# Performance work log

Measured on AMD Instinct MI355X. Metric: run time of the kernel, lower is better.

The kernel has to match this reference:

```python
import jax, jax.numpy as jnp
import numpy as np
from functools import partial

N_SEEDS = 1000       # n
BG_LOW, BG_UP = 0.3, 0.7
ERODE_K, ERODE_ITER = 11, 1
KSZ = 3
IGNORE = -255
INT_MAX = np.iinfo(np.int32).max


def _min_pool2d(x, k):
    # binary erosion with a kxk all-ones structuring element, SAME padding
    return jax.lax.reduce_window(x, INT_MAX, jax.lax.min, (k, k), (1, 1), 'SAME')


def _max_pool3d(x, k):
    # binary dilation over (B,H,W) with kxk window on spatial dims
    return jax.lax.reduce_window(x, -INT_MAX, jax.lax.max, (1, k, k), (1, 1, 1), 'SAME')


def _otsu_threshold(flat255):
    # flat255: int32 pixel values in [0,255]
    hist = jnp.zeros(256, jnp.float32).at[flat255].add(1.0)
    total = jnp.asarray(flat255.shape[0], jnp.float32)
    bins = jnp.arange(256, dtype=jnp.float32)
    w = jnp.cumsum(hist)                 # class-0 pixel count up to bin t
    m = jnp.cumsum(hist * bins)          # class-0 intensity mass up to t
    mT = m[-1]
    denom = w * (total - w)
    sigma_b = jnp.where(denom > 0, (mT * w - total * m) ** 2 / (denom * total * total), 0.0)
    th = jnp.argmax(sigma_b).astype(jnp.float32)
    bad = jnp.sum(hist > 0) <= 1         # degenerate histogram -> bad_egg
    return th, bad


def _sample_mask(eligible, key, hw):
    # uniform sampling without replacement of min(N_SEEDS, #eligible)
    # via random-score top-k restricted to eligible positions
    scores = jnp.where(eligible, jax.random.uniform(key, (hw,)), -jnp.inf)
    vals, idx = jax.lax.top_k(scores, N_SEEDS)
    sel = (vals > -jnp.inf).astype(jnp.int32)
    return jnp.zeros(hw, jnp.int32).at[idx].max(sel)


def _one_sample(cam, key):
    h, w = cam.shape
    hw = h * w
    cam255 = jnp.floor(cam * 255.0)
    flat255 = jnp.clip(cam255.astype(jnp.int32).ravel(), 0, 255)

    th, bad = _otsu_threshold(flat255)
    th = jnp.where(bad, jnp.median(cam * 255.0), th)
    th = jnp.where(th == 0, 1.0, jnp.where(th == 255, 254.0, th))

    roi = (cam255 > th).astype(jnp.int32)
    for _ in range(ERODE_ITER):
        roi = _min_pool2d(roi, ERODE_K)

    kf, kb, kz = jax.random.split(key, 3)
    # foreground: sample uniformly from eroded ROI pixels
    fg = _sample_mask(roi.ravel() == 1, kf, hw)
    # background: sample uniformly from the nbr_bg lowest-activation pixels
    z = jax.random.uniform(kz, (), minval=BG_LOW, maxval=BG_UP)
    nbr_bg = jnp.ceil(z * hw)
    order = jnp.argsort(cam.ravel())
    rank = jnp.zeros(hw, jnp.int32).at[order].set(jnp.arange(hw, dtype=jnp.int32))
    bg = _sample_mask(rank.astype(jnp.float32) < nbr_bg, kb, hw)
    return fg.reshape(h, w), bg.reshape(h, w)


def setup_inputs() -> dict:
    key = jax.random.key(0)
    x = jax.random.uniform(key, (128, 1, 512, 512), dtype=jnp.float32)
    return {"x": x}


def reference(x):
    b, d, h, w = x.shape
    keys = jax.random.split(jax.random.key(42), b)
    all_fg, all_bg = jax.vmap(_one_sample)(x[:, 0], keys)   # (B,H,W) int32
    # dilation with ksz x ksz ones kernel
    all_fg = _max_pool3d(all_fg, KSZ)
    all_bg = _max_pool3d(all_bg, KSZ)
    outer = all_fg + all_bg
    all_fg = jnp.where(outer == 2, 0, all_fg)
    all_bg = jnp.where(outer == 2, 0, all_bg)
    out = jnp.full((b, h, w), IGNORE, dtype=jnp.int32)
    out = jnp.where(all_fg == 1, 1, out)
    out = jnp.where(all_bg == 1, 0, out)
    return out
```

## Files before the change

kernel.cpp:

```cpp
#include <hip/hip_runtime.h>
#include <cstdint>

typedef unsigned short u16;

constexpr int BATCH = 128;
constexpr int H = 512, W = 512;
constexpr int HW = H * W;
constexpr int WPR = W / 64;
constexpr int WPI = HW / 64;
constexpr int NSEED = 1000;
constexpr int MARGIN = 3000;
constexpr int CAP2 = 4096;
constexpr int CAPS = 1024;
constexpr int LBUF = 2048;
constexpr int NBIN = 4096;
constexpr int QSEG = 128;

__device__ __forceinline__ uint32_t rotl32(uint32_t v, int d) {
  return (v << d) | (v >> (32 - d));
}

__device__ __forceinline__ void tf2x32(uint32_t k0, uint32_t k1,
                                       uint32_t x0, uint32_t x1,
                                       uint32_t &o0, uint32_t &o1) {
  uint32_t ks2 = k0 ^ k1 ^ 0x1BD11BDAu;
  x0 += k0; x1 += k1;
  x0 += x1; x1 = rotl32(x1, 13); x1 ^= x0;
  x0 += x1; x1 = rotl32(x1, 15); x1 ^= x0;
  x0 += x1; x1 = rotl32(x1, 26); x1 ^= x0;
  x0 += x1; x1 = rotl32(x1, 6);  x1 ^= x0;
  x0 += k1; x1 += ks2 + 1u;
  x0 += x1; x1 = rotl32(x1, 17); x1 ^= x0;
  x0 += x1; x1 = rotl32(x1, 29); x1 ^= x0;
  x0 += x1; x1 = rotl32(x1, 16); x1 ^= x0;
  x0 += x1; x1 = rotl32(x1, 24); x1 ^= x0;
  x0 += ks2; x1 += k0 + 2u;
  x0 += x1; x1 = rotl32(x1, 13); x1 ^= x0;
  x0 += x1; x1 = rotl32(x1, 15); x1 ^= x0;
  x0 += x1; x1 = rotl32(x1, 26); x1 ^= x0;
  x0 += x1; x1 = rotl32(x1, 6);  x1 ^= x0;
  x0 += k0; x1 += k1 + 3u;
  x0 += x1; x1 = rotl32(x1, 17); x1 ^= x0;
  x0 += x1; x1 = rotl32(x1, 29); x1 ^= x0;
  x0 += x1; x1 = rotl32(x1, 16); x1 ^= x0;
  x0 += x1; x1 = rotl32(x1, 24); x1 ^= x0;
  x0 += k1; x1 += ks2 + 4u;
  x0 += x1; x1 = rotl32(x1, 13); x1 ^= x0;
  x0 += x1; x1 = rotl32(x1, 15); x1 ^= x0;
  x0 += x1; x1 = rotl32(x1, 26); x1 ^= x0;
  x0 += x1; x1 = rotl32(x1, 6);  x1 ^= x0;
  x0 += ks2; x1 += k0 + 5u;
  o0 = x0; o1 = x1;
}

__device__ __forceinline__ uint32_t score_bits(uint32_t k0, uint32_t k1, uint32_t i) {
  uint32_t a, c; tf2x32(k0, k1, 0u, i, a, c);
  return a ^ c;
}

__device__ __forceinline__ void keygen(int b, uint32_t* keys, uint32_t* kbg,
                                       uint32_t* Tbg) {
  uint32_t kb0, kb1; tf2x32(0u, 42u, 0u, (uint32_t)b, kb0, kb1);
  uint32_t kf0, kf1; tf2x32(kb0, kb1, 0u, 0u, kf0, kf1);
  uint32_t kB0, kB1; tf2x32(kb0, kb1, 0u, 1u, kB0, kB1);
  uint32_t kz0, kz1; tf2x32(kb0, kb1, 0u, 2u, kz0, kz1);
  uint32_t za, zc; tf2x32(kz0, kz1, 0u, 0u, za, zc);
  uint32_t zb = za ^ zc;
  keys[b * 4 + 0] = kf0; keys[b * 4 + 1] = kf1;
  keys[b * 4 + 2] = kB0; keys[b * 4 + 3] = kB1;
  float uu = __uint_as_float((zb >> 9) | 0x3f800000u) - 1.0f;
  float span = __fsub_rn(0.7f, 0.3f);
  float z = __fadd_rn(__fmul_rn(uu, span), 0.3f);
  z = fmaxf(0.3f, z);
  float nb = ceilf(__fmul_rn(z, (float)HW));
  uint32_t K = (uint32_t)nb;
  kbg[b] = K;
  float tv = floorf((1.0f - (float)MARGIN / (float)K) * 8388608.0f);
  Tbg[b] = (uint32_t)fmaxf(tv, 0.0f);
}

__global__ __launch_bounds__(1024) void k_binify(const float4* __restrict__ x4,
                                                 u16* __restrict__ g,
                                                 uint32_t* __restrict__ gh,
                                                 uint32_t* __restrict__ keys,
                                                 uint32_t* __restrict__ kbg,
                                                 uint32_t* __restrict__ Tbg,
                                                 uint32_t* __restrict__ Efg,
                                                 uint32_t* __restrict__ cnt_fg,
                                                 uint32_t* __restrict__ cnt_be,
                                                 uint32_t* __restrict__ cnt_bg) {
  __shared__ uint32_t h[NBIN];
  int b = blockIdx.x >> 2, sub = blockIdx.x & 3, t = threadIdx.x;
  if (blockIdx.x == 0 && t < BATCH) {
    keygen(t, keys, kbg, Tbg);
    Efg[t] = 0; cnt_fg[t] = 0; cnt_be[t] = 0; cnt_bg[t] = 0;
  }
  for (int i = t; i < NBIN; i += 1024) h[i] = 0;
  __syncthreads();
  const float4* xb = x4 + ((size_t)b * HW + (size_t)sub * (HW / 4)) / 4;
  ushort4* gb4 = (ushort4*)g + ((size_t)b * HW + (size_t)sub * (HW / 4)) / 4;
  for (int i = t; i < HW / 16; i += 1024) {
    float4 v4 = xb[i];
    int g0 = (int)floorf(__fmul_rn(v4.x, 4080.0f)); g0 = min(max(g0, 0), 4079);
    int g1 = (int)floorf(__fmul_rn(v4.y, 4080.0f)); g1 = min(max(g1, 0), 4079);
    int g2 = (int)floorf(__fmul_rn(v4.z, 4080.0f)); g2 = min(max(g2, 0), 4079);
    int g3 = (int)floorf(__fmul_rn(v4.w, 4080.0f)); g3 = min(max(g3, 0), 4079);
    atomicAdd(&h[g0], 1u);
    atomicAdd(&h[g1], 1u);
    atomicAdd(&h[g2], 1u);
    atomicAdd(&h[g3], 1u);
    ushort4 o;
    o.x = (u16)g0; o.y = (u16)g1; o.z = (u16)g2; o.w = (u16)g3;
    gb4[i] = o;
  }
  __syncthreads();
  uint32_t* dst = gh + ((size_t)blockIdx.x << 12);
  for (int i = t; i < NBIN; i += 1024) dst[i] = h[i];
}

__device__ __forceinline__ void lds_tree_cumsum256x2(float* Lc, float* Sc,
                                                     float* Lm, float* Sm, int tid) {
  const int off[9] = {0, 256, 384, 448, 480, 496, 504, 508, 510};
  const int sz[9]  = {256, 128, 64, 32, 16, 8, 4, 2, 1};
  for (int l = 0; l < 8; ++l) {
    int o = off[l], on = off[l + 1], n = sz[l + 1];
    if (tid < n) {
      Lc[on + tid] = __fadd_rn(Lc[o + 2 * tid], Lc[o + 2 * tid + 1]);
      Lm[on + tid] = __fadd_rn(Lm[o + 2 * tid], Lm[o + 2 * tid + 1]);
    }
    __syncthreads();
  }
  if (tid == 0) { Sc[off[8]] = Lc[off[8]]; Sm[off[8]] = Lm[off[8]]; }
  __syncthreads();
  for (int l = 7; l >= 0; --l) {
    int o = off[l], on = off[l + 1], hn = sz[l] / 2;
    if (tid == 0) { Sc[o] = Lc[o]; Sm[o] = Lm[o]; }
    if (tid < hn) { Sc[o + 2 * tid + 1] = Sc[on + tid]; Sm[o + 2 * tid + 1] = Sm[on + tid]; }
    if (tid >= 1 && tid < hn) {
      Sc[o + 2 * tid] = __fadd_rn(Sc[on + tid - 1], Lc[o + 2 * tid]);
      Sm[o + 2 * tid] = __fadd_rn(Sm[on + tid - 1], Lm[o + 2 * tid]);
    }
    __syncthreads();
  }
}

__global__ __launch_bounds__(256) void k_otsu(const uint32_t* __restrict__ gh,
                                              const uint32_t* __restrict__ kbg,
                                              int* __restrict__ th_out,
                                              uint32_t* __restrict__ b1a,
                                              uint32_t* __restrict__ r1a) {
  __shared__ uint32_t h[NBIN];
  __shared__ float Lc[511], Sc[511], Lm[511], Sm[511];
  __shared__ float av[4];
  __shared__ int ai[4];
  int b = blockIdx.x, t = threadIdx.x;
  const uint32_t* g0 = gh + ((size_t)(b * 4 + 0) << 12);
  const uint32_t* g1 = gh + ((size_t)(b * 4 + 1) << 12);
  const uint32_t* g2 = gh + ((size_t)(b * 4 + 2) << 12);
  const uint32_t* g3 = gh + ((size_t)(b * 4 + 3) << 12);
  for (int i = t; i < NBIN; i += 256) h[i] = g0[i] + g1[i] + g2[i] + g3[i];
  __syncthreads();
  uint32_t hv = 0;
#pragma unroll
  for (int i = 0; i < 16; ++i) hv += h[t * 16 + ((i + t) & 15)];
  Lc[t] = (float)hv;
  Lm[t] = __fmul_rn((float)hv, (float)t);
  __syncthreads();
  lds_tree_cumsum256x2(Lc, Sc, Lm, Sm, t);
  uint32_t K = kbg[b];
  {
    float total = (float)HW;
    float mT = Sm[255];
    float w = Sc[t];
    float denom = __fmul_rn(w, __fsub_rn(total, w));
    float s = 0.0f;
    if (denom > 0.0f) {
      float d  = __fsub_rn(__fmul_rn(mT, w), __fmul_rn(total, Sm[t]));
      float nu = __fmul_rn(d, d);
      float dd = __fmul_rn(__fmul_rn(denom, total), total);
      s = __fdiv_rn(nu, dd);
    }
    float bv = s; int bidx = t;
#pragma unroll
    for (int d = 32; d >= 1; d >>= 1) {
      float ov = __shfl_xor(bv, d, 64);
      int oi = __shfl_xor(bidx, d, 64);
      if (ov > bv || (ov == bv && oi < bidx)) { bv = ov; bidx = oi; }
    }
    if ((t & 63) == 0) { av[t >> 6] = bv; ai[t >> 6] = bidx; }
    bool gf = (Sc[t] >= (float)K) && (t == 0 || Sc[t - 1] < (float)K);
    if (gf) {
      uint32_t accv = (t == 0) ? 0u : (uint32_t)Sc[t - 1];
      uint32_t b1v = 0, r1v = 1;
      for (int bin = t * 16; bin < t * 16 + 16; ++bin) {
        uint32_t cc = h[bin];
        if (accv + cc >= K) { b1v = (uint32_t)bin; r1v = K - accv; break; }
        accv += cc;
      }
      b1a[b] = b1v; r1a[b] = r1v;
    }
  }
  __syncthreads();
  if (t == 0) {
    float bv = av[0]; int bidx = ai[0];
#pragma unroll
    for (int wv = 1; wv < 4; ++wv) {
      float ov = av[wv]; int oi = ai[wv];
      if (ov > bv || (ov == bv && oi < bidx)) { bv = ov; bidx = oi; }
    }
    int bi = bidx;
    if (bi == 0) bi = 1;
    if (bi == 255) bi = 254;
    th_out[b] = bi;
  }
}

__global__ __launch_bounds__(1024) void k_main(const u16* __restrict__ gq,
                                               const float* __restrict__ x,
                                               const int* __restrict__ th,
                                               const uint32_t* __restrict__ b1a,
                                               const uint32_t* __restrict__ Tbg,
                                               const uint32_t* __restrict__ keys,
                                               uint32_t* __restrict__ Efg,
                                               uint32_t* __restrict__ cnt_bg,
                                               uint64_t* __restrict__ list,
                                               uint32_t* __restrict__ cnt_be,
                                               uint64_t* __restrict__ list_be,
                                               uint64_t* __restrict__ erod) {
  __shared__ uint64_t sroi[1104];
  __shared__ uint64_t srow[1104];
  __shared__ uint64_t lbuf[LBUF];
  __shared__ uint32_t wq[16 * QSEG];
  __shared__ uint32_t lcnt, gbase;
  int b = blockIdx.x >> 2, sub = blockIdx.x & 3, t = threadIdx.x;
  int wave = t >> 6, lane = t & 63;
  int R0 = sub * 128;
  int rlo = max(R0 - 5, 0), rhi = min(R0 + 133, H);
  int nwords = (rhi - rlo) * 8;
  const u16* gb = gq + (size_t)b * HW;
  const float* xb = x + (size_t)b * HW;
  int groi = (th[b] + 1) << 4;
  uint32_t b1 = b1a[b];
  uint32_t T = Tbg[b];
  uint32_t k0 = keys[b * 4 + 2], k1 = keys[b * 4 + 3];
  if (t == 0) lcnt = 0;
  __syncthreads();
  uint32_t* q = wq + wave * QSEG;
  uint32_t qlen = 0, hd = 0;
  uint64_t lmask = (1ull << lane) - 1ull;
  for (int r = 0; r < 8; ++r) {
    int absr = R0 + wave * 8 + r;
    int rowbase = absr * W + lane;
    int swbase = (absr - rlo) * 8;
    const u16* gp8 = gb + rowbase;
    u16 gvals[8];
#pragma unroll
    for (int c = 0; c < 8; ++c) gvals[c] = gp8[c * 64];
#pragma unroll
    for (int c = 0; c < 8; ++c) {
      uint32_t gv = (uint32_t)gvals[c];
      uint64_t bw = __ballot((int)gv >= groi);
      if (lane == 0) sroi[swbase + c] = bw;
      bool elig = gv < b1;
      uint64_t m = __ballot(elig);
      if (elig) {
        uint32_t rank = (uint32_t)__popcll(m & lmask);
        uint32_t idx = hd + qlen + rank;
        if (idx >= (uint32_t)QSEG) idx -= (uint32_t)QSEG;
        q[idx] = (uint32_t)(rowbase + c * 64);
      }
      qlen += (uint32_t)__popcll(m);
      if (gv == b1) {
        uint32_t gp = atomicAdd(&cnt_be[b], 1u);
        if (gp < (uint32_t)CAPS)
          list_be[(size_t)b * CAPS + gp] =
              (((uint64_t)__float_as_uint(xb[rowbase + c * 64])) << 18) |
              (uint32_t)(rowbase + c * 64);
      }
      while (qlen >= 64u) {
        __builtin_amdgcn_wave_barrier();
        uint32_t idx = hd + (uint32_t)lane;
        if (idx >= (uint32_t)QSEG) idx -= (uint32_t)QSEG;
        uint32_t p = q[idx];
        hd += 64u; if (hd >= (uint32_t)QSEG) hd -= (uint32_t)QSEG;
        qlen -= 64u;
        uint32_t v = score_bits(k0, k1, p) >> 9;
        if (v >= T) {
          uint32_t pos = atomicAdd(&lcnt, 1u);
          uint64_t key = (((uint64_t)((~v) & 0x7FFFFFu)) << 18) | p;
          if (pos < (uint32_t)LBUF) lbuf[pos] = key;
          else { uint32_t gp = atomicAdd(&cnt_bg[b], 1u);
                 if (gp < (uint32_t)CAP2) list[(size_t)b * CAP2 + gp] = key; }
        }
      }
    }
  }
  if (qlen) {
    __builtin_amdgcn_wave_barrier();
    if ((uint32_t)lane < qlen) {
      uint32_t idx = hd + (uint32_t)lane;
      if (idx >= (uint32_t)QSEG) idx -= (uint32_t)QSEG;
      uint32_t p = q[idx];
      uint32_t v = score_bits(k0, k1, p) >> 9;
      if (v >= T) {
        uint32_t pos = atomicAdd(&lcnt, 1u);
        uint64_t key = (((uint64_t)((~v) & 0x7FFFFFu)) << 18) | p;
        if (pos < (uint32_t)LBUF) lbuf[pos] = key;
        else { uint32_t gp = atomicAdd(&cnt_bg[b], 1u);
               if (gp < (uint32_t)CAP2) list[(size_t)b * CAP2 + gp] = key; }
      }
    }
  }
  {
    int lowWords = (R0 - rlo) * 8;
    int nh = nwords - 1024;
    for (int i = wave; i < nh; i += 16) {
      int wi = i + ((i < lowWords) ? 0 : 1024);
      int absr = rlo + (wi >> 3);
      int c = wi & 7;
      uint32_t gv = (uint32_t)gb[absr * W + c * 64 + lane];
      uint64_t bw = __ballot((int)gv >= groi);
      if (lane == 0) sroi[wi] = bw;
    }
  }
  __syncthreads();
  for (int wi = t; wi < nwords; wi += 1024) {
    int c = wi & 7;
    uint64_t cur = sroi[wi];
    uint64_t left  = (c > 0) ? sroi[wi - 1] : ~0ull;
    uint64_t right = (c < 7) ? sroi[wi + 1] : ~0ull;
    uint64_t res = cur;
#pragma unroll
    for (int s = 1; s <= 5; ++s) {
      res &= (cur >> s) | (right << (64 - s));
      res &= (cur << s) | (left >> (64 - s));
    }
    srow[wi] = res;
  }
  __syncthreads();
  {
    int coreRow = t >> 3, c = t & 7;
    int absr = R0 + coreRow;
    int s = absr - rlo;
    uint64_t res = srow[s * 8 + c];
#pragma unroll
    for (int d = 1; d <= 5; ++d) {
      if (absr - d >= 0) res &= srow[(s - d) * 8 + c];
      if (absr + d < H)  res &= srow[(s + d) * 8 + c];
    }
    erod[(size_t)b * WPI + absr * 8 + c] = res;
    uint32_t pc = (uint32_t)__popcll(res);
    for (int sh = 32; sh >= 1; sh >>= 1) pc += __shfl_down(pc, sh);
    if (lane == 0 && pc) atomicAdd(&Efg[b], pc);
  }
  __syncthreads();
  int m = min((int)lcnt, LBUF);
  if (t == 0) gbase = atomicAdd(&cnt_bg[b], (uint32_t)m);
  __syncthreads();
  uint32_t base = gbase;
  for (int i = t; i < m; i += 1024) {
    uint32_t pos = base + (uint32_t)i;
    if (pos < (uint32_t)CAP2) list[(size_t)b * CAP2 + pos] = lbuf[i];
  }
}

__global__ __launch_bounds__(1024) void k_selcomp(const uint32_t* __restrict__ r1a,
                                                  const uint32_t* __restrict__ cnt_be,
                                                  const uint64_t* __restrict__ list_be,
                                                  const uint32_t* __restrict__ Tbg,
                                                  const uint32_t* __restrict__ keys,
                                                  const uint32_t* __restrict__ cnt_bg,
                                                  const uint64_t* __restrict__ list,
                                                  const uint32_t* __restrict__ Ea,
                                                  uint32_t* __restrict__ cnt_fg,
                                                  uint64_t* __restrict__ list_fg,
                                                  const uint64_t* __restrict__ bmE,
                                                  int* __restrict__ out) {
  __shared__ uint64_t Gbit[WPI];
  __shared__ uint64_t Fbit[WPI];
  __shared__ uint64_t pool[5248];
  __shared__ uint32_t ecnt, tcnt, lcnt, gbase, sb2, sr2;
  int b = blockIdx.x, t = threadIdx.x;
  uint32_t* G32 = (uint32_t*)Gbit;
  uint32_t* F32 = (uint32_t*)Fbit;
  uint32_t* h = (uint32_t*)(pool + 2048);
  uint64_t* tie = pool + 4096;
  uint32_t* S = (uint32_t*)(pool + 5120);
  for (int i = t; i < WPI; i += 1024) { Gbit[i] = 0; Fbit[i] = 0; }
  if (t == 0) { ecnt = 0; tcnt = 0; }

  {
    uint64_t* ks = pool;
    uint64_t* ebuf = pool + 1024;
    int nbe = min((int)cnt_be[b], CAPS);
    if (t < nbe) ks[t] = list_be[(size_t)b * CAPS + t];
    __syncthreads();
    if (t < nbe) {
      uint64_t mk = ks[t];
      int rank = 0;
      for (int i = 0; i < nbe; ++i) rank += (ks[i] < mk) ? 1 : 0;
      int r = min((int)r1a[b], nbe);
      if (rank < r) {
        uint32_t p = (uint32_t)(mk & 0x3FFFFull);
        uint32_t v = score_bits(keys[b * 4 + 2], keys[b * 4 + 3], p) >> 9;
        if (v >= Tbg[b]) {
          uint32_t slot = atomicAdd(&ecnt, 1u);
          ebuf[slot] = (((uint64_t)((~v) & 0x7FFFFFu)) << 18) | p;
        }
      }
    }
    for (int i = t; i < 4096; i += 1024) h[i] = 0;
    __syncthreads();
    int n0 = min((int)cnt_bg[b], CAP2);
    int ne = (int)ecnt;
    int n = n0 + ne;
    if (n > 0) {
      uint32_t target = (uint32_t)min(NSEED, n);
      const uint64_t* lb = list + (size_t)b * CAP2;
      uint64_t K0 = (t < n0)        ? lb[t]        : 0;
      uint64_t K1 = (t + 1024 < n0) ? lb[t + 1024] : 0;
      uint64_t K2 = (t + 2048 < n0) ? lb[t + 2048] : 0;
      uint64_t K3 = (t + 3072 < n0) ? lb[t + 3072] : 0;
      uint64_t KE = (t < ne)        ? ebuf[t]      : 0;
      if (t < n0)        atomicAdd(&h[(uint32_t)(K0 >> 29)], 1u);
      if (t + 1024 < n0) atomicAdd(&h[(uint32_t)(K1 >> 29)], 1u);
      if (t + 2048 < n0) atomicAdd(&h[(uint32_t)(K2 >> 29)], 1u);
      if (t + 3072 < n0) atomicAdd(&h[(uint32_t)(K3 >> 29)], 1u);
      if (t < ne)        atomicAdd(&h[(uint32_t)(KE >> 29)], 1u);
      __syncthreads();
      if (t < 256) {
        uint32_t s = 0;
#pragma unroll
        for (int i = 0; i < 16; ++i) s += h[t * 16 + ((i + t) & 15)];
        S[t] = s;
      }
      __syncthreads();
      for (int st = 1; st < 256; st <<= 1) {
        uint32_t v = 0;
        if (t < 256 && t >= st) v = S[t - st];
        __syncthreads();
        if (t < 256) S[t] += v;
        __syncthreads();
      }
      if (t < 256) {
        uint32_t before = (t == 0) ? 0u : S[t - 1];
        if (S[t] >= target && before < target) {
          uint32_t acc = before;
          for (int i = 0; i < 16; ++i) {
            uint32_t c = h[t * 16 + i];
            if (acc + c >= target) { sb2 = (uint32_t)(t * 16 + i); sr2 = target - acc; break; }
            acc += c;
          }
        }
      }
      __syncthreads();
      uint32_t b2 = sb2, r2 = sr2;
#define PROCB(KK, VALID) \
      if (VALID) { \
        uint32_t bin = (uint32_t)((KK) >> 29); \
        if (bin < b2) { \
          uint32_t p = (uint32_t)(KK) & 0x3FFFFu; \
          atomicOr(&G32[p >> 5], 1u << (p & 31)); \
        } else if (bin == b2) { \
          uint32_t pos = atomicAdd(&tcnt, 1u); \
          if (pos < 1024u) tie[pos] = (KK); \
        } \
      }
      PROCB(K0, t < n0) PROCB(K1, t + 1024 < n0) PROCB(K2, t + 2048 < n0)
      PROCB(K3, t + 3072 < n0) PROCB(KE, t < ne)
#undef PROCB
      __syncthreads();
      int m = min((int)tcnt, 1024);
      int r = min((int)r2, m);
      if (t < m) {
        uint64_t mk = tie[t];
        int rank = 0;
        for (int i = 0; i < m; ++i) rank += (tie[i] < mk) ? 1 : 0;
        if (rank < r) {
          uint32_t p = (uint32_t)mk & 0x3FFFFu;
          atomicOr(&G32[p >> 5], 1u << (p & 31));
        }
      }
    }
  }
  __syncthreads();

  {
    uint32_t E = Ea[b];
    const uint64_t* eb = bmE + (size_t)b * WPI;
    if (E <= (uint32_t)NSEED) {
      for (int i = t; i < WPI; i += 1024) Fbit[i] = eb[i];
      __syncthreads();
    } else {
      uint64_t* lbuf = pool;
      if (t == 0) { lcnt = 0; tcnt = 0; }
      for (int i = t; i < 4096; i += 1024) h[i] = 0;
      __syncthreads();
      float tvf = floorf((1.0f - (float)MARGIN / (float)E) * 8388608.0f);
      uint32_t T = (uint32_t)fmaxf(tvf, 0.0f);
      uint32_t k0 = keys[b * 4 + 0], k1 = keys[b * 4 + 1];
      int lane = t & 63;
      for (int k = 0; k < HW / 1024; ++k) {
        uint32_t p = (uint32_t)(k * 1024 + t);
        uint64_t wbits = eb[p >> 6];
        if ((wbits >> lane) & 1ull) {
          uint32_t v = score_bits(k0, k1, p) >> 9;
          if (v >= T) {
            uint32_t pos = atomicAdd(&lcnt, 1u);
            uint64_t key = (((uint64_t)((~v) & 0x7FFFFFu)) << 18) | p;
            if (pos < (uint32_t)LBUF) lbuf[pos] = key;
            else { uint32_t gp = atomicAdd(&cnt_fg[b], 1u);
                   if (gp < (uint32_t)CAP2) list_fg[(size_t)b * CAP2 + gp] = key; }
          }
        }
      }
      __syncthreads();
      int m2 = min((int)lcnt, LBUF);
      if (t == 0) gbase = atomicAdd(&cnt_fg[b], (uint32_t)m2);
      __syncthreads();
      for (int i = t; i < m2; i += 1024) {
        uint32_t pos = gbase + (uint32_t)i;
        if (pos < (uint32_t)CAP2) list_fg[(size_t)b * CAP2 + pos] = lbuf[i];
      }
      __syncthreads();
      int n = min((int)cnt_fg[b], CAP2);
      if (n > 0) {
        uint32_t target = (uint32_t)min(NSEED, n);
        const uint64_t* lb = list_fg + (size_t)b * CAP2;
        uint64_t K0 = (t < n)        ? lb[t]        : 0;
        uint64_t K1 = (t + 1024 < n) ? lb[t + 1024] : 0;
        uint64_t K2 = (t + 2048 < n) ? lb[t + 2048] : 0;
        uint64_t K3 = (t + 3072 < n) ? lb[t + 3072] : 0;
        if (t < n)        atomicAdd(&h[(uint32_t)(K0 >> 29)], 1u);
        if (t + 1024 < n) atomicAdd(&h[(uint32_t)(K1 >> 29)], 1u);
        if (t + 2048 < n) atomicAdd(&h[(uint32_t)(K2 >> 29)], 1u);
        if (t + 3072 < n) atomicAdd(&h[(uint32_t)(K3 >> 29)], 1u);
        __syncthreads();
        if (t < 256) {
          uint32_t s = 0;
#pragma unroll
          for (int i = 0; i < 16; ++i) s += h[t * 16 + ((i + t) & 15)];
          S[t] = s;
        }
        __syncthreads();
        for (int st = 1; st < 256; st <<= 1) {
          uint32_t v = 0;
          if (t < 256 && t >= st) v = S[t - st];
          __syncthreads();
          if (t < 256) S[t] += v;
          __syncthreads();
        }
        if (t < 256) {
          uint32_t before = (t == 0) ? 0u : S[t - 1];
          if (S[t] >= target && before < target) {
            uint32_t acc = before;
            for (int i = 0; i < 16; ++i) {
              uint32_t c = h[t * 16 + i];
              if (acc + c >= target) { sb2 = (uint32_t)(t * 16 + i); sr2 = target - acc; break; }
              acc += c;
            }
          }
        }
        __syncthreads();
        uint32_t b2 = sb2, r2 = sr2;
#define PROCF(KK, VALID) \
        if (VALID) { \
          uint32_t bin = (uint32_t)((KK) >> 29); \
          if (bin < b2) { \
            uint32_t p = (uint32_t)(KK) & 0x3FFFFu; \
            atomicOr(&F32[p >> 5], 1u << (p & 31)); \
          } else if (bin == b2) { \
            uint32_t pos = atomicAdd(&tcnt, 1u); \
            if (pos < 1024u) tie[pos] = (KK); \
          } \
        }
        PROCF(K0, t < n) PROCF(K1, t + 1024 < n) PROCF(K2, t + 2048 < n)
        PROCF(K3, t + 3072 < n)
#undef PROCF
        __syncthreads();
        int m = min((int)tcnt, 1024);
        int r = min((int)r2, m);
        if (t < m) {
          uint64_t mk = tie[t];
          int rank = 0;
          for (int i = 0; i < m; ++i) rank += (tie[i] < mk) ? 1 : 0;
          if (rank < r) {
            uint32_t p = (uint32_t)mk & 0x3FFFFu;
            atomicOr(&F32[p >> 5], 1u << (p & 31));
          }
        }
      }
      __syncthreads();
    }
  }
  __syncthreads();

  uint64_t* FdS = pool;
  uint64_t* BdS = pool + 512;
  for (int it = 0; it < 8; ++it) {
    {
      int s = t >> 7, xx = t & 127;
      int w = xx & 63;
      int rg = it * 8 + s;
      int r = rg * 8 + (w >> 3), c = w & 7;
      const uint64_t* src = (xx < 64) ? Fbit : Gbit;
      uint64_t d = 0;
#pragma unroll
      for (int dr = -1; dr <= 1; ++dr) {
        int rr = r + dr;
        if (rr < 0 || rr >= H) continue;
        int wi = rr * 8 + c;
        uint64_t cur = src[wi];
        uint64_t lf = (c > 0) ? src[wi - 1] : 0ull;
        uint64_t rt = (c < 7) ? src[wi + 1] : 0ull;
        d |= cur | (cur << 1) | (lf >> 63) | (cur >> 1) | (rt << 63);
      }
      if (xx < 64) FdS[s * 64 + w] = d; else BdS[s * 64 + w] = d;
    }
    __syncthreads();
    int4* ob = (int4*)out + (size_t)b * (HW / 4) + (size_t)it * 8192;
#pragma unroll
    for (int k2 = 0; k2 < 8; ++k2) {
      int idx = k2 * 1024 + t;
      int ss = idx >> 10, i = idx & 1023;
      int ww = i >> 4, sub = i & 15;
      uint64_t Fd = FdS[ss * 64 + ww], Bd = BdS[ss * 64 + ww];
      uint64_t ov = Fd & Bd;
      Fd &= ~ov; Bd &= ~ov;
      int sh = sub * 4;
      int4 o;
      o.x = ((Fd >> (sh + 0)) & 1ull) ? 1 : (((Bd >> (sh + 0)) & 1ull) ? 0 : -255);
      o.y = ((Fd >> (sh + 1)) & 1ull) ? 1 : (((Bd >> (sh + 1)) & 1ull) ? 0 : -255);
      o.z = ((Fd >> (sh + 2)) & 1ull) ? 1 : (((Bd >> (sh + 2)) & 1ull) ? 0 : -255);
      o.w = ((Fd >> (sh + 3)) & 1ull) ? 1 : (((Bd >> (sh + 3)) & 1ull) ? 0 : -255);
      ob[idx] = o;
    }
    __syncthreads();
  }
}

extern "C" void kernel_launch(void* const* d_in, const int* in_sizes, int n_in,
                              void* d_out, int out_size, void* d_ws, size_t ws_size,
                              hipStream_t stream) {
  (void)in_sizes; (void)n_in; (void)out_size; (void)ws_size;
  const float* x = (const float*)d_in[0];
  int* out = (int*)d_out;
  char* ws = (char*)d_ws;

  u16* g = (u16*)d_out;

  uint32_t* keys   = (uint32_t*)(ws + 0);
  uint32_t* kbg    = (uint32_t*)(ws + 2048);
  int*      th     = (int*)     (ws + 2560);
  uint32_t* b1a    = (uint32_t*)(ws + 3072);
  uint32_t* r1a    = (uint32_t*)(ws + 3584);
  uint32_t* Tbg    = (uint32_t*)(ws + 4096);
  uint32_t* Efg    = (uint32_t*)(ws + 4608);
  uint32_t* cnt_fg = (uint32_t*)(ws + 5120);
  uint32_t* cnt_be = (uint32_t*)(ws + 5632);
  uint32_t* cnt_bg = (uint32_t*)(ws + 6144);
  uint32_t* gh      = (uint32_t*)(ws + 8192);
  uint64_t* list    = (uint64_t*)(ws + 8192 + 8388608);
  uint64_t* list_be = (uint64_t*)(ws + 8192 + 8388608 + 4194304);
  uint64_t* bmE     = (uint64_t*)(ws + 8192 + 8388608 + 5242880);
  uint64_t* list_fg = (uint64_t*)gh;

  k_binify  <<<BATCH * 4, 1024, 0, stream>>>((const float4*)x, g, gh, keys, kbg,
                                             Tbg, Efg, cnt_fg, cnt_be, cnt_bg);
  k_otsu    <<<BATCH, 256, 0, stream>>>(gh, kbg, th, b1a, r1a);
  k_main    <<<BATCH * 4, 1024, 0, stream>>>(g, x, th, b1a, Tbg, keys,
                                             Efg, cnt_bg, list, cnt_be, list_be, bmE);
  k_selcomp <<<BATCH, 1024, 0, stream>>>(r1a, cnt_be, list_be, Tbg, keys,
                                         cnt_bg, list, Efg, cnt_fg, list_fg,
                                         bmE, out);
}
```

Before: 339.3 us.

## Split selection/compose kernel across two blocks per image and double queue drain width

k_selcomp now launches two blocks per image. Each block redundantly performs the full fg/bg selection, with separate fg counters and lists per half so the two blocks do not collide, then writes only its half of the output rows. This doubles the number of blocks working on the write-heavy compose phase at the cost of duplicated selection work. In k_main the eligibility queue grows to 256 entries and is drained 128 items at a time, two per lane, to add instruction-level parallelism in the hash scoring. A 64-wide tail drain handles leftovers.

Result: no change. 335.6 us (-1.1%).

```diff
diff --git a/kernel.cpp b/kernel.cpp
--- a/kernel.cpp
+++ b/kernel.cpp
@@ -14,7 +14,7 @@
 constexpr int CAPS = 1024;
 constexpr int LBUF = 2048;
 constexpr int NBIN = 4096;
-constexpr int QSEG = 128;
+constexpr int QSEG = 256;
 
 __device__ __forceinline__ uint32_t rotl32(uint32_t v, int d) {
   return (v << d) | (v >> (32 - d));
@@ -93,8 +93,9 @@
   int b = blockIdx.x >> 2, sub = blockIdx.x & 3, t = threadIdx.x;
   if (blockIdx.x == 0 && t < BATCH) {
     keygen(t, keys, kbg, Tbg);
-    Efg[t] = 0; cnt_fg[t] = 0; cnt_be[t] = 0; cnt_bg[t] = 0;
-  }
+    Efg[t] = 0; cnt_be[t] = 0; cnt_bg[t] = 0;
+  }
+  if (blockIdx.x == 0 && t < 2 * BATCH) cnt_fg[t] = 0;
   for (int i = t; i < NBIN; i += 1024) h[i] = 0;
   __syncthreads();
   const float4* xb = x4 + ((size_t)b * HW + (size_t)sub * (HW / 4)) / 4;
@@ -277,22 +278,49 @@
               (((uint64_t)__float_as_uint(xb[rowbase + c * 64])) << 18) |
               (uint32_t)(rowbase + c * 64);
       }
-      while (qlen >= 64u) {
+      while (qlen >= 128u) {
         __builtin_amdgcn_wave_barrier();
-        uint32_t idx = hd + (uint32_t)lane;
-        if (idx >= (uint32_t)QSEG) idx -= (uint32_t)QSEG;
-        uint32_t p = q[idx];
-        hd += 64u; if (hd >= (uint32_t)QSEG) hd -= (uint32_t)QSEG;
-        qlen -= 64u;
-        uint32_t v = score_bits(k0, k1, p) >> 9;
-        if (v >= T) {
+        uint32_t i0 = hd + (uint32_t)lane;
+        if (i0 >= (uint32_t)QSEG) i0 -= (uint32_t)QSEG;
+        uint32_t i1 = hd + 64u + (uint32_t)lane;
+        if (i1 >= (uint32_t)QSEG) i1 -= (uint32_t)QSEG;
+        uint32_t p0 = q[i0];
+        uint32_t p1 = q[i1];
+        hd += 128u; if (hd >= (uint32_t)QSEG) hd -= (uint32_t)QSEG;
+        qlen -= 128u;
+        uint32_t v0 = score_bits(k0, k1, p0) >> 9;
+        uint32_t v1 = score_bits(k0, k1, p1) >> 9;
+        if (v0 >= T) {
           uint32_t pos = atomicAdd(&lcnt, 1u);
-          uint64_t key = (((uint64_t)((~v) & 0x7FFFFFu)) << 18) | p;
+          uint64_t key = (((uint64_t)((~v0) & 0x7FFFFFu)) << 18) | p0;
           if (pos < (uint32_t)LBUF) lbuf[pos] = key;
           else { uint32_t gp = atomicAdd(&cnt_bg[b], 1u);
                  if (gp < (uint32_t)CAP2) list[(size_t)b * CAP2 + gp] = key; }
         }
-      }
+        if (v1 >= T) {
+          uint32_t pos = atomicAdd(&lcnt, 1u);
+          uint64_t key = (((uint64_t)((~v1) & 0x7FFFFFu)) << 18) | p1;
+          if (pos < (uint32_t)LBUF) lbuf[pos] = key;
+          else { uint32_t gp = atomicAdd(&cnt_bg[b], 1u);
+                 if (gp < (uint32_t)CAP2) list[(size_t)b * CAP2 + gp] = key; }
+        }
+      }
+    }
+  }
+  while (qlen >= 64u) {
+    __builtin_amdgcn_wave_barrier();
+    uint32_t idx = hd + (uint32_t)lane;
+    if (idx >= (uint32_t)QSEG) idx -= (uint32_t)QSEG;
+    uint32_t p = q[idx];
+    hd += 64u; if (hd >= (uint32_t)QSEG) hd -= (uint32_t)QSEG;
+    qlen -= 64u;
+    uint32_t v = score_bits(k0, k1, p) >> 9;
+    if (v >= T) {
+      uint32_t pos = atomicAdd(&lcnt, 1u);
+      uint64_t key = (((uint64_t)((~v) & 0x7FFFFFu)) << 18) | p;
+      if (pos < (uint32_t)LBUF) lbuf[pos] = key;
+      else { uint32_t gp = atomicAdd(&cnt_bg[b], 1u);
+             if (gp < (uint32_t)CAP2) list[(size_t)b * CAP2 + gp] = key; }
     }
   }
   if (qlen) {
@@ -380,7 +408,8 @@
   __shared__ uint64_t Fbit[WPI];
   __shared__ uint64_t pool[5248];
   __shared__ uint32_t ecnt, tcnt, lcnt, gbase, sb2, sr2;
-  int b = blockIdx.x, t = threadIdx.x;
+  int b = blockIdx.x >> 1, sub = blockIdx.x & 1, t = threadIdx.x;
+  int bsub = b * 2 + sub;
   uint32_t* G32 = (uint32_t*)Gbit;
   uint32_t* F32 = (uint32_t*)Fbit;
   uint32_t* h = (uint32_t*)(pool + 2048);
@@ -509,24 +538,24 @@
             uint32_t pos = atomicAdd(&lcnt, 1u);
             uint64_t key = (((uint64_t)((~v) & 0x7FFFFFu)) << 18) | p;
             if (pos < (uint32_t)LBUF) lbuf[pos] = key;
-            else { uint32_t gp = atomicAdd(&cnt_fg[b], 1u);
-                   if (gp < (uint32_t)CAP2) list_fg[(size_t)b * CAP2 + gp] = key; }
+            else { uint32_t gp = atomicAdd(&cnt_fg[bsub], 1u);
+                   if (gp < (uint32_t)CAP2) list_fg[(size_t)bsub * CAP2 + gp] = key; }
           }
         }
       }
       __syncthreads();
       int m2 = min((int)lcnt, LBUF);
-      if (t == 0) gbase = atomicAdd(&cnt_fg[b], (uint32_t)m2);
+      if (t == 0) gbase = atomicAdd(&cnt_fg[bsub], (uint32_t)m2);
       __syncthreads();
       for (int i = t; i < m2; i += 1024) {
         uint32_t pos = gbase + (uint32_t)i;
-        if (pos < (uint32_t)CAP2) list_fg[(size_t)b * CAP2 + pos] = lbuf[i];
-      }
-      __syncthreads();
-      int n = min((int)cnt_fg[b], CAP2);
+        if (pos < (uint32_t)CAP2) list_fg[(size_t)bsub * CAP2 + pos] = lbuf[i];
+      }
+      __syncthreads();
+      int n = min((int)cnt_fg[bsub], CAP2);
       if (n > 0) {
         uint32_t target = (uint32_t)min(NSEED, n);
-        const uint64_t* lb = list_fg + (size_t)b * CAP2;
+        const uint64_t* lb = list_fg + (size_t)bsub * CAP2;
         uint64_t K0 = (t < n)        ? lb[t]        : 0;
         uint64_t K1 = (t + 1024 < n) ? lb[t + 1024] : 0;
         uint64_t K2 = (t + 2048 < n) ? lb[t + 2048] : 0;
@@ -597,11 +626,11 @@
 
   uint64_t* FdS = pool;
   uint64_t* BdS = pool + 512;
-  for (int it = 0; it < 8; ++it) {
+  for (int it = 0; it < 4; ++it) {
     {
       int s = t >> 7, xx = t & 127;
       int w = xx & 63;
-      int rg = it * 8 + s;
+      int rg = sub * 32 + it * 8 + s;
       int r = rg * 8 + (w >> 3), c = w & 7;
       const uint64_t* src = (xx < 64) ? Fbit : Gbit;
       uint64_t d = 0;
@@ -618,16 +647,17 @@
       if (xx < 64) FdS[s * 64 + w] = d; else BdS[s * 64 + w] = d;
     }
     __syncthreads();
-    int4* ob = (int4*)out + (size_t)b * (HW / 4) + (size_t)it * 8192;
+    int4* ob = (int4*)out + (size_t)b * (HW / 4) + (size_t)sub * (HW / 8)
+             + (size_t)it * 8192;
 #pragma unroll
     for (int k2 = 0; k2 < 8; ++k2) {
       int idx = k2 * 1024 + t;
       int ss = idx >> 10, i = idx & 1023;
-      int ww = i >> 4, sub = i & 15;
+      int ww = i >> 4, sub4 = i & 15;
       uint64_t Fd = FdS[ss * 64 + ww], Bd = BdS[ss * 64 + ww];
       uint64_t ov = Fd & Bd;
       Fd &= ~ov; Bd &= ~ov;
-      int sh = sub * 4;
+      int sh = sub4 * 4;
       int4 o;
       o.x = ((Fd >> (sh + 0)) & 1ull) ? 1 : (((Bd >> (sh + 0)) & 1ull) ? 0 : -255);
       o.y = ((Fd >> (sh + 1)) & 1ull) ? 1 : (((Bd >> (sh + 1)) & 1ull) ? 0 : -255);
@@ -656,9 +686,9 @@
   uint32_t* r1a    = (uint32_t*)(ws + 3584);
   uint32_t* Tbg    = (uint32_t*)(ws + 4096);
   uint32_t* Efg    = (uint32_t*)(ws + 4608);
-  uint32_t* cnt_fg = (uint32_t*)(ws + 5120);
-  uint32_t* cnt_be = (uint32_t*)(ws + 5632);
-  uint32_t* cnt_bg = (uint32_t*)(ws + 6144);
+  uint32_t* cnt_be = (uint32_t*)(ws + 5120);
+  uint32_t* cnt_bg = (uint32_t*)(ws + 5632);
+  uint32_t* cnt_fg = (uint32_t*)(ws + 6144);
   uint32_t* gh      = (uint32_t*)(ws + 8192);
   uint64_t* list    = (uint64_t*)(ws + 8192 + 8388608);
   uint64_t* list_be = (uint64_t*)(ws + 8192 + 8388608 + 4194304);
@@ -670,7 +700,7 @@
   k_otsu    <<<BATCH, 256, 0, stream>>>(gh, kbg, th, b1a, r1a);
   k_main    <<<BATCH * 4, 1024, 0, stream>>>(g, x, th, b1a, Tbg, keys,
                                              Efg, cnt_bg, list, cnt_be, list_be, bmE);
-  k_selcomp <<<BATCH, 1024, 0, stream>>>(r1a, cnt_be, list_be, Tbg, keys,
-                                         cnt_bg, list, Efg, cnt_fg, list_fg,
-                                         bmE, out);
-}
+  k_selcomp <<<BATCH * 2, 1024, 0, stream>>>(r1a, cnt_be, list_be, Tbg, keys,
+                                             cnt_bg, list, Efg, cnt_fg, list_fg,
+                                             bmE, out);
+}
```
